# Optimization experiments

Measured on AMD Instinct MI355X. Metric: run time of the kernel, lower is better.

The kernel has to match this reference:

```python
import jax, jax.numpy as jnp
import numpy as np

H = 512  # h_dim = d_rnn


def _pair_mlp(paragraph, W1, W2):
    """Fused equivalent of: cat(p_i, p_j) @ W1 -> ReLU -> @ W2 -> ReLU.
    Splits W1 so the [B,n,n,2h] concatenated input is never materialized
    before the first GEMM.  paragraph: [B, n, H]; W1: [2H, 2H]; W2: [2H, d_pair].
    Returns [B, n, n, d_pair].
    """
    u = paragraph @ W1[:H]   # [B, n, 2H]  (contribution of p_i, broadcast over j)
    v = paragraph @ W1[H:]   # [B, n, 2H]  (contribution of p_j, broadcast over i)
    z = jax.nn.relu(u[:, :, None, :] + v[:, None, :, :])  # [B, n, n, 2H]
    return jax.nn.relu(z @ W2)  # [B, n, n, d_pair]  (dropout = identity in eval)


def reference(paragraph, Wf1, Wf2, w3, Wh1a, Wh1b, wl1, Wh2a, Wh2b, wl2):
    # rela_encode -> future MLP, then directional probs via w3
    rela_vec = _pair_mlp(paragraph, Wf1, Wf2)            # [B,n,n,d_pair]
    rela_p = jax.nn.softmax(rela_vec @ w3, axis=-1)      # [B,n,n,2]
    rela_vec_diret = jnp.concatenate((rela_vec, rela_p), axis=-1)

    # encode_history -> hist_left1 / hist_left2 MLPs and their heads
    hist1 = _pair_mlp(paragraph, Wh1a, Wh1b)
    hist2 = _pair_mlp(paragraph, Wh2a, Wh2b)
    left1_p = jax.nn.softmax(hist1 @ wl1, axis=-1)
    left2_p = jax.nn.softmax(hist2 @ wl2, axis=-1)
    hist_vec_left1 = jnp.concatenate((hist1, left1_p), axis=-1)
    hist_vec_left2 = jnp.concatenate((hist2, left2_p), axis=-1)

    # pack all rela_pred outputs into one tensor: [B, n, n, 3*(d_pair+2)]
    return jnp.concatenate((rela_vec_diret, hist_vec_left1, hist_vec_left2), axis=-1)


def setup_inputs() -> dict:
    key = jax.random.key(0)
    ks = jax.random.split(key, 10)
    B, N, d_pair = 4, 128, 256
    s1 = 1.0 / np.sqrt(2 * H)
    s2 = 1.0 / np.sqrt(d_pair)
    return {
        "paragraph": jax.random.normal(ks[0], (B, N, H), jnp.float32),
        "Wf1": jax.random.normal(ks[1], (2 * H, 2 * H), jnp.float32) * s1,
        "Wf2": jax.random.normal(ks[2], (2 * H, d_pair), jnp.float32) * s1,
        "w3": jax.random.normal(ks[3], (d_pair, 2), jnp.float32) * s2,
        "Wh1a": jax.random.normal(ks[4], (2 * H, 2 * H), jnp.float32) * s1,
        "Wh1b": jax.random.normal(ks[5], (2 * H, d_pair), jnp.float32) * s1,
        "wl1": jax.random.normal(ks[6], (d_pair, 2), jnp.float32) * s2,
        "Wh2a": jax.random.normal(ks[7], (2 * H, 2 * H), jnp.float32) * s1,
        "Wh2b": jax.random.normal(ks[8], (2 * H, d_pair), jnp.float32) * s1,
        "wl2": jax.random.normal(ks[9], (d_pair, 2), jnp.float32) * s2,
    }
```

## Files before the change

### kernel.cpp

```cpp
#include <hip/hip_runtime.h>


typedef __attribute__((ext_vector_type(4))) float floatx4;
typedef __attribute__((ext_vector_type(2))) float floatx2;
typedef __attribute__((ext_vector_type(8))) short short8;

#define KT 16
#define LSTRIDE 68

__device__ __forceinline__ void gload_lds16(const void* g, void* l) {
  __builtin_amdgcn_global_load_lds(
      (const __attribute__((address_space(1))) void*)g,
      (__attribute__((address_space(3))) void*)l, 16, 0, 0);
}

__device__ __forceinline__ void split8(const float* x, short8& hi, short8& lo) {
  unsigned hb[8], lb[8];
#pragma unroll
  for (int e = 0; e < 8; e++) {
    unsigned xb = __float_as_uint(x[e]);
    unsigned h = xb & 0xFFFF0000u;
    float l = x[e] - __uint_as_float(h);
    hb[e] = h;
    lb[e] = __float_as_uint(l) & 0xFFFF0000u;
  }
  union U { unsigned u[4]; short8 s; };
  U H, L;
#pragma unroll
  for (int p = 0; p < 4; p++) {
    H.u[p] = __builtin_amdgcn_perm(hb[2 * p + 1], hb[2 * p], 0x07060302u);
    L.u[p] = __builtin_amdgcn_perm(lb[2 * p + 1], lb[2 * p], 0x07060302u);
  }
  hi = H.s;
  lo = L.s;
}

__global__ __launch_bounds__(256) void prep_w1f(
    const float* __restrict__ W1,
    unsigned short* __restrict__ W1F) {
  int t = blockIdx.x * 256 + threadIdx.x;
  int lane = t & 63;
  int nf = (t >> 6) & 127;
  int kt = t >> 13;
  int g = lane >> 4, c = lane & 15;
  int n = nf * 16 + c;
  int kbase = kt * 32 + g * 8;
  const float* src = W1 + (long)((n >= 1024 ? 512 : 0) + kbase) * 1024 + (n & 1023);

  unsigned hb[8], lb[8];
#pragma unroll
  for (int e = 0; e < 8; e++) {
    float w = src[(long)e * 1024];
    unsigned wb = __float_as_uint(w);
    unsigned h = wb & 0xFFFF0000u;
    float l = w - __uint_as_float(h);
    hb[e] = h;
    lb[e] = __float_as_uint(l) & 0xFFFF0000u;
  }
  union U { unsigned u[4]; short8 s; };
  U H, L;
#pragma unroll
  for (int p = 0; p < 4; p++) {
    H.u[p] = __builtin_amdgcn_perm(hb[2 * p + 1], hb[2 * p], 0x07060302u);
    L.u[p] = __builtin_amdgcn_perm(lb[2 * p + 1], lb[2 * p], 0x07060302u);
  }
  long base = ((long)kt * 128 + nf) * 2 * 64 + lane;
  *(short8*)(W1F + (base + 0) * 8) = H.s;
  *(short8*)(W1F + (base + 64) * 8) = L.s;
}

__global__ __launch_bounds__(256) void stage1_mfma(
    const float* __restrict__ P,
    const unsigned short* __restrict__ W1F,
    float* __restrict__ uv) {
  int bx = blockIdx.x;
  int m0 = (bx >> 4) * 16;
  int n0 = (bx & 15) * 128;
  int tid = threadIdx.x;
  int wid = tid >> 6, lane = tid & 63;
  int g = lane >> 4, r = lane & 15;
  int nw0 = n0 + wid * 32;

  const float* prow = P + (long)(m0 + r) * 512;

  floatx4 acc[2];
#pragma unroll
  for (int nf = 0; nf < 2; nf++) acc[nf] = (floatx4){0.f, 0.f, 0.f, 0.f};

  for (int kt = 0; kt < 16; kt++) {
    int k0 = kt * 32 + g * 8;
    float a[8];
    floatx4 a0 = *(const floatx4*)(prow + k0);
    floatx4 a1 = *(const floatx4*)(prow + k0 + 4);
#pragma unroll
    for (int e = 0; e < 4; e++) { a[e] = a0[e]; a[4 + e] = a1[e]; }
    short8 ahi, alo;
    split8(a, ahi, alo);
#pragma unroll
    for (int nf = 0; nf < 2; nf++) {
      int nfg = (nw0 >> 4) + nf;
      const unsigned short* wp = W1F + (((long)kt * 128 + nfg) * 2 * 64 + lane) * 8;
      short8 whi = *(const short8*)wp;
      short8 wlo = *(const short8*)(wp + 64 * 8);
      acc[nf] = __builtin_amdgcn_mfma_f32_16x16x32_bf16(ahi, whi, acc[nf], 0, 0, 0);
      acc[nf] = __builtin_amdgcn_mfma_f32_16x16x32_bf16(alo, whi, acc[nf], 0, 0, 0);
      acc[nf] = __builtin_amdgcn_mfma_f32_16x16x32_bf16(ahi, wlo, acc[nf], 0, 0, 0);
    }
  }
#pragma unroll
  for (int nf = 0; nf < 2; nf++)
#pragma unroll
    for (int reg = 0; reg < 4; reg++)
      uv[(long)(m0 + g * 4 + reg) * 2048 + nw0 + nf * 16 + r] = acc[nf][reg];
}

__global__ __launch_bounds__(256) void stage1_valu(
    const float* __restrict__ P,
    const float* __restrict__ W1,
    float* __restrict__ uv) {
  __shared__ float at[KT][LSTRIDE];
  __shared__ float wt[KT][LSTRIDE];
  int bx = blockIdx.x;
  int m0 = (bx >> 5) * 64;
  int c0 = (bx & 31) * 64;
  int half = c0 >> 10;
  int ccol = c0 & 1023;
  int tid = threadIdx.x;
  int tm = tid >> 4, tn = tid & 15;
  int lm = tid >> 2;
  int lk4 = (tid & 3) * 4;
  int lkk = tid >> 4;
  int lc4 = (tid & 15) * 4;

  float acc[4][4] = {};

  for (int k0 = 0; k0 < 512; k0 += KT) {
    floatx4 pa = *(const floatx4*)(P + (long)(m0 + lm) * 512 + k0 + lk4);
    floatx4 wa = *(const floatx4*)(W1 + (long)(half * 512 + k0 + lkk) * 1024 + ccol + lc4);
    __syncthreads();
#pragma unroll
    for (int e = 0; e < 4; e++) at[lk4 + e][lm] = pa[e];
    *(floatx4*)&wt[lkk][lc4] = wa;
    __syncthreads();
#pragma unroll
    for (int kk = 0; kk < KT; kk++) {
      floatx4 av = *(const floatx4*)&at[kk][tm * 4];
      floatx4 wv = *(const floatx4*)&wt[kk][tn * 4];
#pragma unroll
      for (int mm = 0; mm < 4; mm++)
#pragma unroll
        for (int nn = 0; nn < 4; nn++)
          acc[mm][nn] += av[mm] * wv[nn];
    }
  }
#pragma unroll
  for (int mm = 0; mm < 4; mm++) {
    floatx4 o;
#pragma unroll
    for (int nn = 0; nn < 4; nn++) o[nn] = acc[mm][nn];
    *(floatx4*)(uv + (long)(m0 + tm * 4 + mm) * 2048 + c0 + tn * 4) = o;
  }
}

__global__ __launch_bounds__(256) void prep_w2(
    const float* __restrict__ W2,
    unsigned short* __restrict__ W2F) {
  int t = blockIdx.x * 256 + threadIdx.x;
  int lane = t & 63;
  int nf = (t >> 6) & 15;
  int kt = t >> 10;
  int g = lane >> 4, c = lane & 15;
  int n = nf * 16 + c;
  int kbase = kt * 32 + g * 8;

  unsigned hb[8], lb[8];
#pragma unroll
  for (int e = 0; e < 8; e++) {
    float w = W2[(long)(kbase + e) * 256 + n];
    unsigned wb = __float_as_uint(w);
    unsigned h = wb & 0xFFFF0000u;
    float l = w - __uint_as_float(h);
    hb[e] = h;
    lb[e] = __float_as_uint(l) & 0xFFFF0000u;
  }
  union U { unsigned u[4]; short8 s; };
  U H, L;
#pragma unroll
  for (int p = 0; p < 4; p++) {
    H.u[p] = __builtin_amdgcn_perm(hb[2 * p + 1], hb[2 * p], 0x07060302u);
    L.u[p] = __builtin_amdgcn_perm(lb[2 * p + 1], lb[2 * p], 0x07060302u);
  }
  long base = (((long)kt * 16 + nf) * 2) * 64 + lane;
  *(short8*)(W2F + (base + 0) * 8) = H.s;
  *(short8*)(W2F + (base + 64) * 8) = L.s;
}

__device__ __forceinline__ void make_frag(
    const floatx4& ua, const floatx4& ub,
    const floatx4& va, const floatx4& vb,
    short8& hi, short8& lo) {
  float z[8];
#pragma unroll
  for (int e = 0; e < 4; e++) {
    z[e] = fmaxf(ua[e] + va[e], 0.0f);
    z[4 + e] = fmaxf(ub[e] + vb[e], 0.0f);
  }
  split8(z, hi, lo);
}

__global__ __launch_bounds__(512, 4) void pair_mfma(
    const float* __restrict__ uv,
    const unsigned short* __restrict__ W2F,
    const float* __restrict__ w3,
    float* __restrict__ out, int mlp) {
  __shared__ unsigned short wbuf[2][16384];
  int bi = blockIdx.x;
  int b = bi >> 7;
  int tid = threadIdx.x;
  int wid = tid >> 6;
  int lane = tid & 63;
  int jq = wid >> 1;
  int nh = wid & 1;
  int g = lane >> 4;
  int r = lane & 15;
  int wj = jq * 32;

  const float* ubase = uv + (long)bi * 2048;
  const float* v0 = uv + (long)(b * 128 + wj + r) * 2048 + 1024;
  const float* v1 = v0 + 16 * 2048;

  floatx4 acc[2][8];
#pragma unroll
  for (int mm = 0; mm < 2; mm++)
#pragma unroll
    for (int nf = 0; nf < 8; nf++) acc[mm][nf] = (floatx4){0.f, 0.f, 0.f, 0.f};

#pragma unroll
  for (int i = 0; i < 4; i++)
    gload_lds16(W2F + (i * 512 + tid) * 8, &wbuf[0][(i * 512 + tid) * 8]);
  __syncthreads();

  int cur = 0;
  for (int kt = 0; kt < 32; kt++) {
    if (kt < 31) {
      const unsigned short* gs = W2F + (long)(kt + 1) * 16384;
#pragma unroll
      for (int i = 0; i < 4; i++)
        gload_lds16(gs + (i * 512 + tid) * 8, &wbuf[cur ^ 1][(i * 512 + tid) * 8]);
    }

    int k0 = kt * 32 + g * 8;
    floatx4 u0  = *(const floatx4*)(ubase + k0);
    floatx4 u1  = *(const floatx4*)(ubase + k0 + 4);
    floatx4 va0 = *(const floatx4*)(v0 + k0);
    floatx4 va1 = *(const floatx4*)(v0 + k0 + 4);
    floatx4 vb0 = *(const floatx4*)(v1 + k0);
    floatx4 vb1 = *(const floatx4*)(v1 + k0 + 4);

    short8 ahi[2], alo[2];
    make_frag(u0, u1, va0, va1, ahi[0], alo[0]);
    make_frag(u0, u1, vb0, vb1, ahi[1], alo[1]);

#pragma unroll
    for (int nf = 0; nf < 8; nf++) {
      int nfg = nh * 8 + nf;
      const unsigned short* wp = &wbuf[cur][(nfg * 2) * 512 + lane * 8];
      short8 whi = *(const short8*)wp;
      short8 wlo = *(const short8*)(wp + 512);
#pragma unroll
      for (int mm = 0; mm < 2; mm++) {
        acc[mm][nf] = __builtin_amdgcn_mfma_f32_16x16x32_bf16(
            ahi[mm], whi, acc[mm][nf], 0, 0, 0);
        acc[mm][nf] = __builtin_amdgcn_mfma_f32_16x16x32_bf16(
            alo[mm], whi, acc[mm][nf], 0, 0, 0);
        acc[mm][nf] = __builtin_amdgcn_mfma_f32_16x16x32_bf16(
            ahi[mm], wlo, acc[mm][nf], 0, 0, 0);
      }
    }
    __syncthreads();
    cur ^= 1;
  }

  float* ps = (float*)wbuf;
  float* ob = out + (long)(bi * 128) * 774 + mlp * 258;
  floatx2 w3v[8];
#pragma unroll
  for (int nf = 0; nf < 8; nf++)
    w3v[nf] = *(const floatx2*)(w3 + ((nh * 8 + nf) * 16 + r) * 2);
#pragma unroll
  for (int mm = 0; mm < 2; mm++) {
    int jrow = wj + mm * 16 + g * 4;
#pragma unroll
    for (int reg = 0; reg < 4; reg++) {
      float* orow = ob + (long)(jrow + reg) * 774 + nh * 128;
      float s0 = 0.f, s1 = 0.f;
#pragma unroll
      for (int nf = 0; nf < 8; nf++) {
        float y = acc[mm][nf][reg];
        y = y > 0.f ? y : 0.f;
        orow[nf * 16 + r] = y;
        s0 += y * w3v[nf][0];
        s1 += y * w3v[nf][1];
      }
#pragma unroll
      for (int off = 1; off < 16; off <<= 1) {
        s0 += __shfl_xor(s0, off, 64);
        s1 += __shfl_xor(s1, off, 64);
      }
      if (r == 0) {
        int row = jrow + reg;
        ps[(row * 2 + nh) * 2 + 0] = s0;
        ps[(row * 2 + nh) * 2 + 1] = s1;
      }
    }
  }
  __syncthreads();
  if (nh == 1 && lane < 32) {
    int row = wj + lane;
    float s0 = ps[(row * 2) * 2 + 0] + ps[(row * 2 + 1) * 2 + 0];
    float s1 = ps[(row * 2) * 2 + 1] + ps[(row * 2 + 1) * 2 + 1];
    float m = fmaxf(s0, s1);
    float e0 = __expf(s0 - m), e1 = __expf(s1 - m);
    float inv = 1.0f / (e0 + e1);
    floatx2 pr;
    pr[0] = e0 * inv;
    pr[1] = e1 * inv;
    *(floatx2*)(ob + (long)row * 774 + 256) = pr;
  }
}

__global__ __launch_bounds__(256) void pair_valu(
    const float* __restrict__ uv,
    const float* __restrict__ W2,
    float* __restrict__ out, int mlp) {
  __shared__ float zt[KT][LSTRIDE];
  __shared__ float wt[KT][LSTRIDE];
  int bx = blockIdx.x;
  int nb = bx & 3;
  int jh = (bx >> 2) & 1;
  int bi = bx >> 3;
  int b = bi >> 7;
  int j0 = jh * 64;
  int n0 = nb * 64;
  int tid = threadIdx.x;
  int tm = tid >> 4, tn = tid & 15;
  int lj = tid >> 2;
  int lk4 = (tid & 3) * 4;
  int lkk = tid >> 4;
  int ln4 = (tid & 15) * 4;

  const float* urow = uv + (long)bi * 2048;
  const float* vrow = uv + (long)(b * 128 + j0 + lj) * 2048 + 1024;

  float acc[4][4] = {};

  for (int k0 = 0; k0 < 1024; k0 += KT) {
    floatx4 uu = *(const floatx4*)(urow + k0 + lk4);
    floatx4 vv = *(const floatx4*)(vrow + k0 + lk4);
    floatx4 wa = *(const floatx4*)(W2 + (long)(k0 + lkk) * 256 + n0 + ln4);
    __syncthreads();
#pragma unroll
    for (int e = 0; e < 4; e++) {
      float z = uu[e] + vv[e];
      zt[lk4 + e][lj] = z > 0.f ? z : 0.f;
    }
    *(floatx4*)&wt[lkk][ln4] = wa;
    __syncthreads();
#pragma unroll
    for (int kk = 0; kk < KT; kk++) {
      floatx4 zv = *(const floatx4*)&zt[kk][tm * 4];
      floatx4 wv = *(const floatx4*)&wt[kk][tn * 4];
#pragma unroll
      for (int mm = 0; mm < 4; mm++)
#pragma unroll
        for (int nn = 0; nn < 4; nn++)
          acc[mm][nn] += zv[mm] * wv[nn];
    }
  }
  float* ob = out + (long)(bi * 128 + j0) * 774 + mlp * 258 + n0 + tn * 4;
#pragma unroll
  for (int mm = 0; mm < 4; mm++) {
    float* orow = ob + (long)(tm * 4 + mm) * 774;
    floatx2 pa, pb;
    pa[0] = acc[mm][0] > 0.f ? acc[mm][0] : 0.f;
    pa[1] = acc[mm][1] > 0.f ? acc[mm][1] : 0.f;
    pb[0] = acc[mm][2] > 0.f ? acc[mm][2] : 0.f;
    pb[1] = acc[mm][3] > 0.f ? acc[mm][3] : 0.f;
    *(floatx2*)orow = pa;
    *(floatx2*)(orow + 2) = pb;
  }
}

__global__ __launch_bounds__(256) void head_kernel(
    const float* __restrict__ w3_0, const float* __restrict__ w3_1,
    const float* __restrict__ w3_2, float* out) {
  int wid = threadIdx.x >> 6, lane = threadIdx.x & 63;
  int r = blockIdx.x * 4 + wid;
  int mlp = r >> 16;
  int row = r & 65535;
  const float* w3 = (mlp == 0) ? w3_0 : (mlp == 1) ? w3_1 : w3_2;
  const float* yp = out + (long)row * 774 + mlp * 258 + lane * 4;
  floatx2 ya = *(const floatx2*)yp;
  floatx2 yb = *(const floatx2*)(yp + 2);
  const float* wp = w3 + lane * 8;
  floatx4 wv0 = *(const floatx4*)wp;
  floatx4 wv1 = *(const floatx4*)(wp + 4);
  float s0 = ya[0] * wv0[0] + ya[1] * wv0[2] + yb[0] * wv1[0] + yb[1] * wv1[2];
  float s1 = ya[0] * wv0[1] + ya[1] * wv0[3] + yb[0] * wv1[1] + yb[1] * wv1[3];
#pragma unroll
  for (int off = 32; off > 0; off >>= 1) {
    s0 += __shfl_xor(s0, off, 64);
    s1 += __shfl_xor(s1, off, 64);
  }
  if (lane == 0) {
    float m = fmaxf(s0, s1);
    float e0 = __expf(s0 - m), e1 = __expf(s1 - m);
    float inv = 1.0f / (e0 + e1);
    floatx2 pr;
    pr[0] = e0 * inv;
    pr[1] = e1 * inv;
    *(floatx2*)(out + (long)row * 774 + mlp * 258 + 256) = pr;
  }
}

extern "C" void kernel_launch(void* const* d_in, const int* in_sizes, int n_in,
                              void* d_out, int out_size, void* d_ws, size_t ws_size,
                              hipStream_t stream) {
  const float* para = (const float*)d_in[0];
  const float* Wf1  = (const float*)d_in[1];
  const float* Wf2  = (const float*)d_in[2];
  const float* w3   = (const float*)d_in[3];
  const float* Wh1a = (const float*)d_in[4];
  const float* Wh1b = (const float*)d_in[5];
  const float* wl1  = (const float*)d_in[6];
  const float* Wh2a = (const float*)d_in[7];
  const float* Wh2b = (const float*)d_in[8];
  const float* wl2  = (const float*)d_in[9];

  float* uv = (float*)d_ws;
  unsigned short* w2f =
      (unsigned short*)((char*)d_ws + (4u << 20));
  unsigned short* w1f =
      (unsigned short*)((char*)d_ws + (5u << 20));
  float* outp = (float*)d_out;

  bool pair_ok   = ws_size >= (size_t)(5u << 20);
  bool stage1_ok = ws_size >= (size_t)(9u << 20);

  const float* W1s[3] = {Wf1, Wh1a, Wh2a};
  const float* W2s[3] = {Wf2, Wh1b, Wh2b};
  const float* w3s[3] = {w3, wl1, wl2};
  for (int mlp = 0; mlp < 3; mlp++) {
    if (stage1_ok) {
      prep_w1f<<<512, 256, 0, stream>>>(W1s[mlp], w1f);
      stage1_mfma<<<512, 256, 0, stream>>>(para, w1f, uv);
    } else {
      stage1_valu<<<256, 256, 0, stream>>>(para, W1s[mlp], uv);
    }
    if (pair_ok) {
      prep_w2<<<128, 256, 0, stream>>>(W2s[mlp], w2f);
      pair_mfma<<<512, 512, 0, stream>>>(uv, w2f, w3s[mlp], outp, mlp);
    } else {
      pair_valu<<<4096, 256, 0, stream>>>(uv, W2s[mlp], outp, mlp);
    }
  }
  if (!pair_ok) head_kernel<<<49152, 256, 0, stream>>>(w3, wl1, wl2, outp);
}
```

Measured before the change: 545.2 us.

## Batch three MLPs into single launches and retile pair kernel to 64x64 warps

Merges the per-MLP weight prep, stage-1 GEMM and pair GEMM launches into three combined launches over all three MLPs, which cuts twelve launches to three and gives each launch more blocks to fill the GPU. The pair kernel's warp tile changes from 32 rows x 128 cols to 64 rows x 64 cols, so each weight fragment read from LDS is reused across four row fragments, and the MFMA section is wrapped in s_setprio. The combined path needs a 27 MB workspace. If the workspace is smaller it falls back to the old per-MLP loop, which now also uses the new pair tiling.

```diff
diff --git a/kernel.cpp b/kernel.cpp
--- a/kernel.cpp
+++ b/kernel.cpp
@@ -7,6 +7,7 @@
 
 #define KT 16
 #define LSTRIDE 68
+#define MB (1u << 20)
 
 __device__ __forceinline__ void gload_lds16(const void* g, void* l) {
   __builtin_amdgcn_global_load_lds(
@@ -35,10 +36,8 @@
   lo = L.s;
 }
 
-__global__ __launch_bounds__(256) void prep_w1f(
-    const float* __restrict__ W1,
-    unsigned short* __restrict__ W1F) {
-  int t = blockIdx.x * 256 + threadIdx.x;
+__device__ __forceinline__ void prep_w1_body(
+    int t, const float* __restrict__ W1, unsigned short* __restrict__ W1F) {
   int lane = t & 63;
   int nf = (t >> 6) & 127;
   int kt = t >> 13;
@@ -69,11 +68,69 @@
   *(short8*)(W1F + (base + 64) * 8) = L.s;
 }
 
-__global__ __launch_bounds__(256) void stage1_mfma(
-    const float* __restrict__ P,
-    const unsigned short* __restrict__ W1F,
-    float* __restrict__ uv) {
+__device__ __forceinline__ void prep_w2_body(
+    int t, const float* __restrict__ W2, unsigned short* __restrict__ W2F) {
+  int lane = t & 63;
+  int nf = (t >> 6) & 15;
+  int kt = t >> 10;
+  int g = lane >> 4, c = lane & 15;
+  int n = nf * 16 + c;
+  int kbase = kt * 32 + g * 8;
+
+  unsigned hb[8], lb[8];
+#pragma unroll
+  for (int e = 0; e < 8; e++) {
+    float w = W2[(long)(kbase + e) * 256 + n];
+    unsigned wb = __float_as_uint(w);
+    unsigned h = wb & 0xFFFF0000u;
+    float l = w - __uint_as_float(h);
+    hb[e] = h;
+    lb[e] = __float_as_uint(l) & 0xFFFF0000u;
+  }
+  union U { unsigned u[4]; short8 s; };
+  U H, L;
+#pragma unroll
+  for (int p = 0; p < 4; p++) {
+    H.u[p] = __builtin_amdgcn_perm(hb[2 * p + 1], hb[2 * p], 0x07060302u);
+    L.u[p] = __builtin_amdgcn_perm(lb[2 * p + 1], lb[2 * p], 0x07060302u);
+  }
+  long base = (((long)kt * 16 + nf) * 2) * 64 + lane;
+  *(short8*)(W2F + (base + 0) * 8) = H.s;
+  *(short8*)(W2F + (base + 64) * 8) = L.s;
+}
+
+__global__ __launch_bounds__(256) void prep_all(
+    const float* __restrict__ Wf1, const float* __restrict__ Wh1a,
+    const float* __restrict__ Wh2a, const float* __restrict__ Wf2,
+    const float* __restrict__ Wh1b, const float* __restrict__ Wh2b,
+    unsigned short* __restrict__ w1f_all, unsigned short* __restrict__ w2f_all) {
   int bx = blockIdx.x;
+  if (bx < 1536) {
+    int mlp = bx >> 9;
+    const float* W1 = (mlp == 0) ? Wf1 : (mlp == 1) ? Wh1a : Wh2a;
+    prep_w1_body((bx & 511) * 256 + threadIdx.x, W1,
+                 w1f_all + (long)mlp * (2 * MB));
+  } else {
+    int bb = bx - 1536;
+    int mlp = bb >> 7;
+    const float* W2 = (mlp == 0) ? Wf2 : (mlp == 1) ? Wh1b : Wh2b;
+    prep_w2_body((bb & 127) * 256 + threadIdx.x, W2,
+                 w2f_all + (long)mlp * (MB / 2));
+  }
+}
+
+__global__ __launch_bounds__(256) void prep_w1f(
+    const float* __restrict__ W1, unsigned short* __restrict__ W1F) {
+  prep_w1_body(blockIdx.x * 256 + threadIdx.x, W1, W1F);
+}
+__global__ __launch_bounds__(256) void prep_w2(
+    const float* __restrict__ W2, unsigned short* __restrict__ W2F) {
+  prep_w2_body(blockIdx.x * 256 + threadIdx.x, W2, W2F);
+}
+
+__device__ __forceinline__ void stage1_core(
+    int bx, const float* __restrict__ P,
+    const unsigned short* __restrict__ W1F, float* __restrict__ uv) {
   int m0 = (bx >> 4) * 16;
   int n0 = (bx & 15) * 128;
   int tid = threadIdx.x;
@@ -114,9 +171,163 @@
       uv[(long)(m0 + g * 4 + reg) * 2048 + nw0 + nf * 16 + r] = acc[nf][reg];
 }
 
+__global__ __launch_bounds__(256) void stage1_mfma(
+    const float* __restrict__ P, const unsigned short* __restrict__ W1F,
+    float* __restrict__ uv) {
+  stage1_core(blockIdx.x, P, W1F, uv);
+}
+
+__global__ __launch_bounds__(256) void stage1_mfma3(
+    const float* __restrict__ P, const unsigned short* __restrict__ w1f_all,
+    float* __restrict__ uv_all) {
+  int mlp = blockIdx.x >> 9;
+  stage1_core(blockIdx.x & 511, P, w1f_all + (long)mlp * (2 * MB),
+              uv_all + (long)mlp * MB);
+}
+
+__device__ __forceinline__ void pair_core(
+    int bi, const float* __restrict__ uv,
+    const unsigned short* __restrict__ W2F, const float* __restrict__ w3,
+    float* __restrict__ out, int mlp, unsigned short (*wbuf)[16384]) {
+  int b = bi >> 7;
+  int tid = threadIdx.x;
+  int wid = tid >> 6;
+  int lane = tid & 63;
+  int jh = wid >> 2;
+  int nq = wid & 3;
+  int g = lane >> 4;
+  int r = lane & 15;
+  int wj = jh * 64;
+
+  const float* ubase = uv + (long)bi * 2048;
+  const float* vbase = uv + (long)(b * 128 + wj + r) * 2048 + 1024;
+
+  floatx4 acc[4][4];
+#pragma unroll
+  for (int mm = 0; mm < 4; mm++)
+#pragma unroll
+    for (int nf = 0; nf < 4; nf++) acc[mm][nf] = (floatx4){0.f, 0.f, 0.f, 0.f};
+
+#pragma unroll
+  for (int i = 0; i < 4; i++)
+    gload_lds16(W2F + (i * 512 + tid) * 8, &wbuf[0][(i * 512 + tid) * 8]);
+  __syncthreads();
+
+  int cur = 0;
+  for (int kt = 0; kt < 32; kt++) {
+    if (kt < 31) {
+      const unsigned short* gs = W2F + (long)(kt + 1) * 16384;
+#pragma unroll
+      for (int i = 0; i < 4; i++)
+        gload_lds16(gs + (i * 512 + tid) * 8, &wbuf[cur ^ 1][(i * 512 + tid) * 8]);
+    }
+
+    int k0 = kt * 32 + g * 8;
+    floatx4 u0 = *(const floatx4*)(ubase + k0);
+    floatx4 u1 = *(const floatx4*)(ubase + k0 + 4);
+    short8 ahi[4], alo[4];
+#pragma unroll
+    for (int mm = 0; mm < 4; mm++) {
+      const float* vr = vbase + (long)mm * 16 * 2048;
+      floatx4 va = *(const floatx4*)(vr + k0);
+      floatx4 vb = *(const floatx4*)(vr + k0 + 4);
+      float z[8];
+#pragma unroll
+      for (int e = 0; e < 4; e++) {
+        z[e]     = fmaxf(u0[e] + va[e], 0.f);
+        z[4 + e] = fmaxf(u1[e] + vb[e], 0.f);
+      }
+      split8(z, ahi[mm], alo[mm]);
+    }
+
+    __builtin_amdgcn_s_setprio(1);
+#pragma unroll
+    for (int nf = 0; nf < 4; nf++) {
+      const unsigned short* wp = &wbuf[cur][((nq * 4 + nf) * 2) * 512 + lane * 8];
+      short8 whi = *(const short8*)wp;
+      short8 wlo = *(const short8*)(wp + 512);
+#pragma unroll
+      for (int mm = 0; mm < 4; mm++) {
+        acc[mm][nf] = __builtin_amdgcn_mfma_f32_16x16x32_bf16(
+            ahi[mm], whi, acc[mm][nf], 0, 0, 0);
+        acc[mm][nf] = __builtin_amdgcn_mfma_f32_16x16x32_bf16(
+            alo[mm], whi, acc[mm][nf], 0, 0, 0);
+        acc[mm][nf] = __builtin_amdgcn_mfma_f32_16x16x32_bf16(
+            ahi[mm], wlo, acc[mm][nf], 0, 0, 0);
+      }
+    }
+    __builtin_amdgcn_s_setprio(0);
+    __syncthreads();
+    cur ^= 1;
+  }
+
+  float* ps = (float*)wbuf;
+  float* ob = out + (long)(bi * 128) * 774 + mlp * 258;
+  floatx2 w3v[4];
+#pragma unroll
+  for (int nf = 0; nf < 4; nf++)
+    w3v[nf] = *(const floatx2*)(w3 + ((nq * 4 + nf) * 16 + r) * 2);
+#pragma unroll
+  for (int mm = 0; mm < 4; mm++) {
+#pragma unroll
+    for (int reg = 0; reg < 4; reg++) {
+      int row = wj + mm * 16 + g * 4 + reg;
+      float* orow = ob + (long)row * 774 + nq * 64;
+      float s0 = 0.f, s1 = 0.f;
+#pragma unroll
+      for (int nf = 0; nf < 4; nf++) {
+        float y = acc[mm][nf][reg];
+        y = y > 0.f ? y : 0.f;
+        orow[nf * 16 + r] = y;
+        s0 += y * w3v[nf][0];
+        s1 += y * w3v[nf][1];
+      }
+#pragma unroll
+      for (int off = 1; off < 16; off <<= 1) {
+        s0 += __shfl_xor(s0, off, 64);
+        s1 += __shfl_xor(s1, off, 64);
+      }
+      if (r == 0) {
+        ps[row * 8 + nq * 2 + 0] = s0;
+        ps[row * 8 + nq * 2 + 1] = s1;
+      }
+    }
+  }
+  __syncthreads();
+  if (tid < 128) {
+    int row = tid;
+    float s0 = ps[row * 8 + 0] + ps[row * 8 + 2] + ps[row * 8 + 4] + ps[row * 8 + 6];
+    float s1 = ps[row * 8 + 1] + ps[row * 8 + 3] + ps[row * 8 + 5] + ps[row * 8 + 7];
+    float m = fmaxf(s0, s1);
+    float e0 = __expf(s0 - m), e1 = __expf(s1 - m);
+    float inv = 1.0f / (e0 + e1);
+    floatx2 pr;
+    pr[0] = e0 * inv;
+    pr[1] = e1 * inv;
+    *(floatx2*)(ob + (long)row * 774 + 256) = pr;
+  }
+}
+
+__global__ __launch_bounds__(512, 4) void pair_mfma(
+    const float* __restrict__ uv, const unsigned short* __restrict__ W2F,
+    const float* __restrict__ w3, float* __restrict__ out, int mlp) {
+  __shared__ unsigned short wbuf[2][16384];
+  pair_core(blockIdx.x, uv, W2F, w3, out, mlp, wbuf);
+}
+
+__global__ __launch_bounds__(512, 4) void pair_mfma3(
+    const float* __restrict__ uv_all, const unsigned short* __restrict__ w2f_all,
+    const float* __restrict__ w3_0, const float* __restrict__ w3_1,
+    const float* __restrict__ w3_2, float* __restrict__ out) {
+  __shared__ unsigned short wbuf[2][16384];
+  int mlp = blockIdx.x >> 9;
+  const float* w3 = (mlp == 0) ? w3_0 : (mlp == 1) ? w3_1 : w3_2;
+  pair_core(blockIdx.x & 511, uv_all + (long)mlp * MB,
+            w2f_all + (long)mlp * (MB / 2), w3, out, mlp, wbuf);
+}
+
 __global__ __launch_bounds__(256) void stage1_valu(
-    const float* __restrict__ P,
-    const float* __restrict__ W1,
+    const float* __restrict__ P, const float* __restrict__ W1,
     float* __restrict__ uv) {
   __shared__ float at[KT][LSTRIDE];
   __shared__ float wt[KT][LSTRIDE];
@@ -162,176 +373,8 @@
   }
 }
 
-__global__ __launch_bounds__(256) void prep_w2(
-    const float* __restrict__ W2,
-    unsigned short* __restrict__ W2F) {
-  int t = blockIdx.x * 256 + threadIdx.x;
-  int lane = t & 63;
-  int nf = (t >> 6) & 15;
-  int kt = t >> 10;
-  int g = lane >> 4, c = lane & 15;
-  int n = nf * 16 + c;
-  int kbase = kt * 32 + g * 8;
-
-  unsigned hb[8], lb[8];
-#pragma unroll
-  for (int e = 0; e < 8; e++) {
-    float w = W2[(long)(kbase + e) * 256 + n];
-    unsigned wb = __float_as_uint(w);
-    unsigned h = wb & 0xFFFF0000u;
-    float l = w - __uint_as_float(h);
-    hb[e] = h;
-    lb[e] = __float_as_uint(l) & 0xFFFF0000u;
-  }
-  union U { unsigned u[4]; short8 s; };
-  U H, L;
-#pragma unroll
-  for (int p = 0; p < 4; p++) {
-    H.u[p] = __builtin_amdgcn_perm(hb[2 * p + 1], hb[2 * p], 0x07060302u);
-    L.u[p] = __builtin_amdgcn_perm(lb[2 * p + 1], lb[2 * p], 0x07060302u);
-  }
-  long base = (((long)kt * 16 + nf) * 2) * 64 + lane;
-  *(short8*)(W2F + (base + 0) * 8) = H.s;
-  *(short8*)(W2F + (base + 64) * 8) = L.s;
-}
-
-__device__ __forceinline__ void make_frag(
-    const floatx4& ua, const floatx4& ub,
-    const floatx4& va, const floatx4& vb,
-    short8& hi, short8& lo) {
-  float z[8];
-#pragma unroll
-  for (int e = 0; e < 4; e++) {
-    z[e] = fmaxf(ua[e] + va[e], 0.0f);
-    z[4 + e] = fmaxf(ub[e] + vb[e], 0.0f);
-  }
-  split8(z, hi, lo);
-}
-
-__global__ __launch_bounds__(512, 4) void pair_mfma(
-    const float* __restrict__ uv,
-    const unsigned short* __restrict__ W2F,
-    const float* __restrict__ w3,
-    float* __restrict__ out, int mlp) {
-  __shared__ unsigned short wbuf[2][16384];
-  int bi = blockIdx.x;
-  int b = bi >> 7;
-  int tid = threadIdx.x;
-  int wid = tid >> 6;
-  int lane = tid & 63;
-  int jq = wid >> 1;
-  int nh = wid & 1;
-  int g = lane >> 4;
-  int r = lane & 15;
-  int wj = jq * 32;
-
-  const float* ubase = uv + (long)bi * 2048;
-  const float* v0 = uv + (long)(b * 128 + wj + r) * 2048 + 1024;
-  const float* v1 = v0 + 16 * 2048;
-
-  floatx4 acc[2][8];
-#pragma unroll
-  for (int mm = 0; mm < 2; mm++)
-#pragma unroll
-    for (int nf = 0; nf < 8; nf++) acc[mm][nf] = (floatx4){0.f, 0.f, 0.f, 0.f};
-
-#pragma unroll
-  for (int i = 0; i < 4; i++)
-    gload_lds16(W2F + (i * 512 + tid) * 8, &wbuf[0][(i * 512 + tid) * 8]);
-  __syncthreads();
-
-  int cur = 0;
-  for (int kt = 0; kt < 32; kt++) {
-    if (kt < 31) {
-      const unsigned short* gs = W2F + (long)(kt + 1) * 16384;
-#pragma unroll
-      for (int i = 0; i < 4; i++)
-        gload_lds16(gs + (i * 512 + tid) * 8, &wbuf[cur ^ 1][(i * 512 + tid) * 8]);
-    }
-
-    int k0 = kt * 32 + g * 8;
-    floatx4 u0  = *(const floatx4*)(ubase + k0);
-    floatx4 u1  = *(const floatx4*)(ubase + k0 + 4);
-    floatx4 va0 = *(const floatx4*)(v0 + k0);
-    floatx4 va1 = *(const floatx4*)(v0 + k0 + 4);
-    floatx4 vb0 = *(const floatx4*)(v1 + k0);
-    floatx4 vb1 = *(const floatx4*)(v1 + k0 + 4);
-
-    short8 ahi[2], alo[2];
-    make_frag(u0, u1, va0, va1, ahi[0], alo[0]);
-    make_frag(u0, u1, vb0, vb1, ahi[1], alo[1]);
-
-#pragma unroll
-    for (int nf = 0; nf < 8; nf++) {
-      int nfg = nh * 8 + nf;
-      const unsigned short* wp = &wbuf[cur][(nfg * 2) * 512 + lane * 8];
-      short8 whi = *(const short8*)wp;
-      short8 wlo = *(const short8*)(wp + 512);
-#pragma unroll
-      for (int mm = 0; mm < 2; mm++) {
-        acc[mm][nf] = __builtin_amdgcn_mfma_f32_16x16x32_bf16(
-            ahi[mm], whi, acc[mm][nf], 0, 0, 0);
-        acc[mm][nf] = __builtin_amdgcn_mfma_f32_16x16x32_bf16(
-            alo[mm], whi, acc[mm][nf], 0, 0, 0);
-        acc[mm][nf] = __builtin_amdgcn_mfma_f32_16x16x32_bf16(
-            ahi[mm], wlo, acc[mm][nf], 0, 0, 0);
-      }
-    }
-    __syncthreads();
-    cur ^= 1;
-  }
-
-  float* ps = (float*)wbuf;
-  float* ob = out + (long)(bi * 128) * 774 + mlp * 258;
-  floatx2 w3v[8];
-#pragma unroll
-  for (int nf = 0; nf < 8; nf++)
-    w3v[nf] = *(const floatx2*)(w3 + ((nh * 8 + nf) * 16 + r) * 2);
-#pragma unroll
-  for (int mm = 0; mm < 2; mm++) {
-    int jrow = wj + mm * 16 + g * 4;
-#pragma unroll
-    for (int reg = 0; reg < 4; reg++) {
-      float* orow = ob + (long)(jrow + reg) * 774 + nh * 128;
-      float s0 = 0.f, s1 = 0.f;
-#pragma unroll
-      for (int nf = 0; nf < 8; nf++) {
-        float y = acc[mm][nf][reg];
-        y = y > 0.f ? y : 0.f;
-        orow[nf * 16 + r] = y;
-        s0 += y * w3v[nf][0];
-        s1 += y * w3v[nf][1];
-      }
-#pragma unroll
-      for (int off = 1; off < 16; off <<= 1) {
-        s0 += __shfl_xor(s0, off, 64);
-        s1 += __shfl_xor(s1, off, 64);
-      }
-      if (r == 0) {
-        int row = jrow + reg;
-        ps[(row * 2 + nh) * 2 + 0] = s0;
-        ps[(row * 2 + nh) * 2 + 1] = s1;
-      }
-    }
-  }
-  __syncthreads();
-  if (nh == 1 && lane < 32) {
-    int row = wj + lane;
-    float s0 = ps[(row * 2) * 2 + 0] + ps[(row * 2 + 1) * 2 + 0];
-    float s1 = ps[(row * 2) * 2 + 1] + ps[(row * 2 + 1) * 2 + 1];
-    float m = fmaxf(s0, s1);
-    float e0 = __expf(s0 - m), e1 = __expf(s1 - m);
-    float inv = 1.0f / (e0 + e1);
-    floatx2 pr;
-    pr[0] = e0 * inv;
-    pr[1] = e1 * inv;
-    *(floatx2*)(ob + (long)row * 774 + 256) = pr;
-  }
-}
-
 __global__ __launch_bounds__(256) void pair_valu(
-    const float* __restrict__ uv,
-    const float* __restrict__ W2,
+    const float* __restrict__ uv, const float* __restrict__ W2,
     float* __restrict__ out, int mlp) {
   __shared__ float zt[KT][LSTRIDE];
   __shared__ float wt[KT][LSTRIDE];
@@ -437,32 +480,44 @@
   const float* Wh2b = (const float*)d_in[8];
   const float* wl2  = (const float*)d_in[9];
 
-  float* uv = (float*)d_ws;
-  unsigned short* w2f =
-      (unsigned short*)((char*)d_ws + (4u << 20));
-  unsigned short* w1f =
-      (unsigned short*)((char*)d_ws + (5u << 20));
   float* outp = (float*)d_out;
-
-  bool pair_ok   = ws_size >= (size_t)(5u << 20);
-  bool stage1_ok = ws_size >= (size_t)(9u << 20);
 
   const float* W1s[3] = {Wf1, Wh1a, Wh2a};
   const float* W2s[3] = {Wf2, Wh1b, Wh2b};
   const float* w3s[3] = {w3, wl1, wl2};
-  for (int mlp = 0; mlp < 3; mlp++) {
-    if (stage1_ok) {
+
+  if (ws_size >= (size_t)27 * MB) {
+    float* uv_all = (float*)d_ws;
+    unsigned short* w2f_all = (unsigned short*)((char*)d_ws + 12 * MB);
+    unsigned short* w1f_all = (unsigned short*)((char*)d_ws + 15 * MB);
+    prep_all<<<1920, 256, 0, stream>>>(Wf1, Wh1a, Wh2a, Wf2, Wh1b, Wh2b,
+                                       w1f_all, w2f_all);
+    stage1_mfma3<<<1536, 256, 0, stream>>>(para, w1f_all, uv_all);
+    pair_mfma3<<<1536, 512, 0, stream>>>(uv_all, w2f_all, w3, wl1, wl2, outp);
+  } else if (ws_size >= (size_t)9 * MB) {
+    float* uv = (float*)d_ws;
+    unsigned short* w2f = (unsigned short*)((char*)d_ws + 4 * MB);
+    unsigned short* w1f = (unsigned short*)((char*)d_ws + 5 * MB);
+    for (int mlp = 0; mlp < 3; mlp++) {
       prep_w1f<<<512, 256, 0, stream>>>(W1s[mlp], w1f);
       stage1_mfma<<<512, 256, 0, stream>>>(para, w1f, uv);
-    } else {
-      stage1_valu<<<256, 256, 0, stream>>>(para, W1s[mlp], uv);
-    }
-    if (pair_ok) {
       prep_w2<<<128, 256, 0, stream>>>(W2s[mlp], w2f);
       pair_mfma<<<512, 512, 0, stream>>>(uv, w2f, w3s[mlp], outp, mlp);
-    } else {
+    }
+  } else if (ws_size >= (size_t)5 * MB) {
+    float* uv = (float*)d_ws;
+    unsigned short* w2f = (unsigned short*)((char*)d_ws + 4 * MB);
+    for (int mlp = 0; mlp < 3; mlp++) {
+      stage1_valu<<<256, 256, 0, stream>>>(para, W1s[mlp], uv);
+      prep_w2<<<128, 256, 0, stream>>>(W2s[mlp], w2f);
+      pair_mfma<<<512, 512, 0, stream>>>(uv, w2f, w3s[mlp], outp, mlp);
+    }
+  } else {
+    float* uv = (float*)d_ws;
+    for (int mlp = 0; mlp < 3; mlp++) {
+      stage1_valu<<<256, 256, 0, stream>>>(para, W1s[mlp], uv);
       pair_valu<<<4096, 256, 0, stream>>>(uv, W2s[mlp], outp, mlp);
     }
-  }
-  if (!pair_ok) head_kernel<<<49152, 256, 0, stream>>>(w3, wl1, wl2, outp);
-}
+    head_kernel<<<49152, 256, 0, stream>>>(w3, wl1, wl2, outp);
+  }
+}
```

Result: slower. 725.3 us (+33.0%).
